# Kernel optimization log

Measured on AMD Instinct MI355X. Metric: run time of the kernel, lower is better.

## Reference

```python
import jax, jax.numpy as jnp
import numpy as np

N = 50000
E = 800000
IN_C = 128
HID = 16
HEADS = 8
OUT_C = 64
NEG_SLOPE = 0.2


def setup_inputs() -> dict:
    key = jax.random.key(0)
    ks = jax.random.split(key, 12)
    x = jax.random.normal(ks[0], (N, IN_C), dtype=jnp.float32)
    edge_index = jax.random.randint(ks[1], (2, E), 0, N, dtype=jnp.int32)
    s = 0.1
    W1 = jax.random.normal(ks[2], (IN_C, HEADS * HID), dtype=jnp.float32) * s
    a1_src = jax.random.normal(ks[3], (HEADS, HID), dtype=jnp.float32) * s
    a1_dst = jax.random.normal(ks[4], (HEADS, HID), dtype=jnp.float32) * s
    b1 = jnp.zeros((HEADS * HID,), dtype=jnp.float32)
    W2 = jax.random.normal(ks[5], (HEADS * HID, OUT_C), dtype=jnp.float32) * s
    a2_src = jax.random.normal(ks[6], (1, OUT_C), dtype=jnp.float32) * s
    a2_dst = jax.random.normal(ks[7], (1, OUT_C), dtype=jnp.float32) * s
    b2 = jnp.zeros((OUT_C,), dtype=jnp.float32)
    return {"x": x, "edge_index": edge_index, "W1": W1, "a1_src": a1_src,
            "a1_dst": a1_dst, "b1": b1, "W2": W2, "a2_src": a2_src,
            "a2_dst": a2_dst, "b2": b2}


def gat_conv(x, src, dst, W, a_src, a_dst, b, heads, ch):
    # linear projection -> [N, H, C]
    h = (x @ W).reshape(N, heads, ch)
    # per-node attention logits [N, H]
    al_s = jnp.einsum('nhc,hc->nh', h, a_src)
    al_d = jnp.einsum('nhc,hc->nh', h, a_dst)
    # per-edge logits [E, H]
    e = jax.nn.leaky_relu(al_s[src] + al_d[dst], NEG_SLOPE)
    # segment softmax over incoming edges of each dst node
    emax = jax.ops.segment_max(e, dst, num_segments=N)
    ee = jnp.exp(e - emax[dst])
    denom = jax.ops.segment_sum(ee, dst, num_segments=N)
    alpha = ee / (denom[dst] + 1e-16)
    # weighted scatter-aggregate of source messages
    msg = h[src] * alpha[:, :, None]  # [E, H, C]
    out = jax.ops.segment_sum(msg, dst, num_segments=N)
    return out.reshape(N, heads * ch) + b


def reference(x, edge_index, W1, a1_src, a1_dst, b1, W2, a2_src, a2_dst, b2):
    # add self loops (PyG GATConv default add_self_loops=True)
    loops = jnp.arange(N, dtype=edge_index.dtype)
    src = jnp.concatenate([edge_index[0], loops])
    dst = jnp.concatenate([edge_index[1], loops])
    h = gat_conv(x, src, dst, W1, a1_src, a1_dst, b1, HEADS, HID)
    h = jax.nn.relu(h)
    # dropout p=0.6 is identity in eval mode
    out = gat_conv(h, src, dst, W2, a2_src, a2_dst, b2, 1, OUT_C)
    return out
```

## Files before the change

### kernel.cpp

```cpp
#include <hip/hip_runtime.h>
#include <hip/hip_fp16.h>
#include <math.h>

#define N_NODES 50000
#define E_EDGES 800000
#define IN_C    128
#define HID     16
#define HEADS   8
#define OUT_C   64
#define NEG_SLOPE 0.2f
#define CELLW   64

typedef _Float16 half8 __attribute__((ext_vector_type(8)));
typedef _Float16 half4 __attribute__((ext_vector_type(4)));
typedef float floatx4 __attribute__((ext_vector_type(4)));

__device__ __forceinline__ float lrelu_exp(float v) {
    v = v > 0.f ? v : NEG_SLOPE * v;
    return __expf(v);
}

__global__ __launch_bounds__(256) void fused_gemm_fill(
    const float* __restrict__ X, const float* __restrict__ W, __half* __restrict__ H,
    const float* __restrict__ a_src, const float* __restrict__ a_dst,
    float* __restrict__ als, float* __restrict__ ald,
    const int* __restrict__ src, const int* __restrict__ dst,
    int* __restrict__ cursor, int* __restrict__ ell) {
    __shared__ _Float16 wT[IN_C * 136];
    const int bid = blockIdx.x;
    const int t = threadIdx.x;

    if (bid & 1) {
        const int tid = (bid >> 1) * 256 + t;
        if (tid < E_EDGES / 4) {
            const int4 s4 = ((const int4*)src)[tid];
            const int4 d4 = ((const int4*)dst)[tid];
            const int p0 = atomicAdd(&cursor[d4.x], 1);
            const int p1 = atomicAdd(&cursor[d4.y], 1);
            const int p2 = atomicAdd(&cursor[d4.z], 1);
            const int p3 = atomicAdd(&cursor[d4.w], 1);
            if (p0 < CELLW) __builtin_nontemporal_store(s4.x, &ell[(size_t)d4.x * CELLW + p0]);
            if (p1 < CELLW) __builtin_nontemporal_store(s4.y, &ell[(size_t)d4.y * CELLW + p1]);
            if (p2 < CELLW) __builtin_nontemporal_store(s4.z, &ell[(size_t)d4.z * CELLW + p2]);
            if (p3 < CELLW) __builtin_nontemporal_store(s4.w, &ell[(size_t)d4.w * CELLW + p3]);
        }
        return;
    }

    {
        const int col = t & 127;
        const int kq = (t >> 7) * 4;
        for (int it = 0; it < 16; ++it) {
            const int k0 = it * 8 + kq;
            half4 hv;
            hv[0] = (_Float16)W[(size_t)(k0 + 0) * IN_C + col];
            hv[1] = (_Float16)W[(size_t)(k0 + 1) * IN_C + col];
            hv[2] = (_Float16)W[(size_t)(k0 + 2) * IN_C + col];
            hv[3] = (_Float16)W[(size_t)(k0 + 3) * IN_C + col];
            *(half4*)&wT[col * 136 + k0] = hv;
        }
    }
    __syncthreads();

    const int wave = t >> 6, lane = t & 63;
    const int m = lane & 15, quad = lane >> 4;
    const int r0w = (bid >> 1) * 64 + wave * 16;
    int rl = r0w + m;
    if (rl >= N_NODES) rl = N_NODES - 1;
    const float* Xr = X + (size_t)rl * IN_C;

    floatx4 acc[8];
#pragma unroll
    for (int i = 0; i < 8; ++i) acc[i] = (floatx4){0.f, 0.f, 0.f, 0.f};

#pragma unroll
    for (int kc = 0; kc < 4; ++kc) {
        const int k8 = kc * 32 + quad * 8;
        const float4 xa = *(const float4*)(Xr + k8);
        const float4 xb = *(const float4*)(Xr + k8 + 4);
        half8 a;
        a[0] = (_Float16)xa.x; a[1] = (_Float16)xa.y;
        a[2] = (_Float16)xa.z; a[3] = (_Float16)xa.w;
        a[4] = (_Float16)xb.x; a[5] = (_Float16)xb.y;
        a[6] = (_Float16)xb.z; a[7] = (_Float16)xb.w;
#pragma unroll
        for (int ct = 0; ct < 8; ++ct) {
            const half8 b = *(const half8*)&wT[(ct * 16 + m) * 136 + k8];
            acc[ct] = __builtin_amdgcn_mfma_f32_16x16x32_f16(a, b, acc[ct], 0, 0, 0);
        }
    }

    _Float16* Hh = (_Float16*)H;
#pragma unroll
    for (int ct = 0; ct < 8; ++ct) {
        const float asv = a_src[ct * 16 + m];
        const float adv = a_dst[ct * 16 + m];
#pragma unroll
        for (int r = 0; r < 4; ++r) {
            const int row = r0w + quad * 4 + r;
            const float c = acc[ct][r];
            float ps = c * asv, pd = c * adv;
            ps += __shfl_xor(ps, 1); pd += __shfl_xor(pd, 1);
            ps += __shfl_xor(ps, 2); pd += __shfl_xor(pd, 2);
            ps += __shfl_xor(ps, 4); pd += __shfl_xor(pd, 4);
            ps += __shfl_xor(ps, 8); pd += __shfl_xor(pd, 8);
            if (row < N_NODES) {
                Hh[(size_t)row * IN_C + ct * 16 + m] = (_Float16)c;
                if (m == 0) {
                    als[(size_t)row * HEADS + ct] = ps;
                    ald[(size_t)row * HEADS + ct] = pd;
                }
            }
        }
    }
}

__global__ __launch_bounds__(256) void agg1_gemm2(
    const int* __restrict__ cnt, const int* __restrict__ ell,
    const float* __restrict__ als, const float* __restrict__ ald,
    const __half* __restrict__ H, const float* __restrict__ b,
    const float* __restrict__ W2, const float* __restrict__ a2_src,
    const float* __restrict__ a2_dst, __half* __restrict__ H2,
    float* __restrict__ als2, float* __restrict__ ald2) {
    __shared__ _Float16 wsh[IN_C * OUT_C];
    __shared__ _Float16 xrowh[32 * 136];
    const int t = threadIdx.x;
    for (int f = t * 4; f < IN_C * OUT_C; f += 1024) {
        const float4 w4 = *(const float4*)&W2[f];
        wsh[f + 0] = (_Float16)w4.x;
        wsh[f + 1] = (_Float16)w4.y;
        wsh[f + 2] = (_Float16)w4.z;
        wsh[f + 3] = (_Float16)w4.w;
    }

    const int nl = t >> 3, h = t & 7;
    int nc = blockIdx.x * 32 + nl;
    if (nc >= N_NODES) nc = N_NODES - 1;
    int deg = cnt[nc];
    deg = deg < CELLW ? deg : CELLW;
    const int* ep = ell + (size_t)nc * CELLW;
    const float ad = ald[nc * HEADS + h];
    float accv[16];
    float ssum;
    {
        const float w = lrelu_exp(als[nc * HEADS + h] + ad);
        const half8* q = (const half8*)(H + ((size_t)nc * HEADS + h) * HID);
        const half8 u0 = q[0], u1 = q[1];
        ssum = w;
#pragma unroll
        for (int j = 0; j < 8; ++j) {
            accv[j] = w * (float)u0[j];
            accv[j + 8] = w * (float)u1[j];
        }
    }
    for (int p = 0; p < deg; p += 4) {
        const int4 s4 = *(const int4*)(ep + p);
        const int s0 = s4.x;
        const int i1 = (p + 1 < deg) ? s4.y : nc;
        const int i2 = (p + 2 < deg) ? s4.z : nc;
        const int i3 = (p + 3 < deg) ? s4.w : nc;
        const float f1 = (p + 1 < deg) ? 1.f : 0.f;
        const float f2 = (p + 2 < deg) ? 1.f : 0.f;
        const float f3 = (p + 3 < deg) ? 1.f : 0.f;
        const float v0 = als[s0 * HEADS + h];
        const float v1 = als[i1 * HEADS + h];
        const float v2 = als[i2 * HEADS + h];
        const float v3 = als[i3 * HEADS + h];
        const half8* q0 = (const half8*)(H + ((size_t)s0 * HEADS + h) * HID);
        const half8* q1 = (const half8*)(H + ((size_t)i1 * HEADS + h) * HID);
        const half8* q2 = (const half8*)(H + ((size_t)i2 * HEADS + h) * HID);
        const half8* q3 = (const half8*)(H + ((size_t)i3 * HEADS + h) * HID);
        const half8 a0 = q0[0], b0 = q0[1];
        const half8 a1 = q1[0], b1 = q1[1];
        const half8 a2 = q2[0], b2 = q2[1];
        const half8 a3 = q3[0], b3 = q3[1];
        const float w0 = lrelu_exp(v0 + ad);
        const float w1 = lrelu_exp(v1 + ad) * f1;
        const float w2 = lrelu_exp(v2 + ad) * f2;
        const float w3 = lrelu_exp(v3 + ad) * f3;
        ssum += (w0 + w1) + (w2 + w3);
#pragma unroll
        for (int j = 0; j < 8; ++j) {
            accv[j]     += w0 * (float)a0[j] + w1 * (float)a1[j] +
                           w2 * (float)a2[j] + w3 * (float)a3[j];
            accv[j + 8] += w0 * (float)b0[j] + w1 * (float)b1[j] +
                           w2 * (float)b2[j] + w3 * (float)b3[j];
        }
    }
    {
        const float inv = 1.f / (ssum + 1e-16f);
        half8 r0, r1;
#pragma unroll
        for (int j = 0; j < 8; ++j) {
            float ra = accv[j] * inv + b[h * 16 + j];
            float rb = accv[j + 8] * inv + b[h * 16 + 8 + j];
            r0[j] = (_Float16)(ra > 0.f ? ra : 0.f);
            r1[j] = (_Float16)(rb > 0.f ? rb : 0.f);
        }
        _Float16* xr = &xrowh[nl * 136 + h * 16];
        *(half8*)(xr) = r0;
        *(half8*)(xr + 8) = r1;
    }

    __syncthreads();

    const int ng = t >> 3, jc = t & 7, j0 = jc * 8;
    const int n2 = blockIdx.x * 32 + ng;
    float o[8] = {};
    const _Float16* xb = &xrowh[ng * 136];
    for (int c8 = 0; c8 < IN_C; c8 += 8) {
        const half8 xv8 = *(const half8*)&xb[c8];
#pragma unroll
        for (int j = 0; j < 8; ++j) {
            const float xv = (float)xv8[j];
            const half8 wv = *(const half8*)&wsh[(c8 + j) * OUT_C + j0];
#pragma unroll
            for (int k = 0; k < 8; ++k) o[k] += xv * (float)wv[k];
        }
    }
    float ps = 0.f, pd = 0.f;
#pragma unroll
    for (int k = 0; k < 8; ++k) {
        ps += o[k] * a2_src[j0 + k];
        pd += o[k] * a2_dst[j0 + k];
    }
    ps += __shfl_xor(ps, 1); pd += __shfl_xor(pd, 1);
    ps += __shfl_xor(ps, 2); pd += __shfl_xor(pd, 2);
    ps += __shfl_xor(ps, 4); pd += __shfl_xor(pd, 4);
    if (n2 < N_NODES) {
        half8 hv;
#pragma unroll
        for (int k = 0; k < 8; ++k) hv[k] = (_Float16)o[k];
        *(half8*)((_Float16*)H2 + (size_t)n2 * OUT_C + j0) = hv;
        if (jc == 0) {
            als2[n2] = ps;
            ald2[n2] = pd;
        }
    }
}

__global__ __launch_bounds__(256) void agg2(
    const int* __restrict__ cnt, const int* __restrict__ ell,
    const float* __restrict__ als, const float* __restrict__ ald,
    const __half* __restrict__ H, const float* __restrict__ b,
    float* __restrict__ out) {
    const int t = threadIdx.x;
    int n = blockIdx.x * 32 + (t >> 3);
    const int j0 = (t & 7) * 8;
    const bool valid = n < N_NODES;
    if (!valid) n = N_NODES - 1;
    int deg = cnt[n];
    deg = deg < CELLW ? deg : CELLW;
    const int* ep = ell + (size_t)n * CELLW;
    const float ad = ald[n];
    float accv[8];
    float ssum;
    {
        const float w = lrelu_exp(als[n] + ad);
        const half8 u = *(const half8*)(H + (size_t)n * OUT_C + j0);
        ssum = w;
#pragma unroll
        for (int k = 0; k < 8; ++k) accv[k] = w * (float)u[k];
    }
    for (int p = 0; p < deg; p += 4) {
        const int4 s4 = *(const int4*)(ep + p);
        const int s0 = s4.x;
        const int i1 = (p + 1 < deg) ? s4.y : n;
        const int i2 = (p + 2 < deg) ? s4.z : n;
        const int i3 = (p + 3 < deg) ? s4.w : n;
        const float f1 = (p + 1 < deg) ? 1.f : 0.f;
        const float f2 = (p + 2 < deg) ? 1.f : 0.f;
        const float f3 = (p + 3 < deg) ? 1.f : 0.f;
        const float v0 = als[s0];
        const float v1 = als[i1];
        const float v2 = als[i2];
        const float v3 = als[i3];
        const half8 u0 = *(const half8*)(H + (size_t)s0 * OUT_C + j0);
        const half8 u1 = *(const half8*)(H + (size_t)i1 * OUT_C + j0);
        const half8 u2 = *(const half8*)(H + (size_t)i2 * OUT_C + j0);
        const half8 u3 = *(const half8*)(H + (size_t)i3 * OUT_C + j0);
        const float w0 = lrelu_exp(v0 + ad);
        const float w1 = lrelu_exp(v1 + ad) * f1;
        const float w2 = lrelu_exp(v2 + ad) * f2;
        const float w3 = lrelu_exp(v3 + ad) * f3;
        ssum += (w0 + w1) + (w2 + w3);
#pragma unroll
        for (int k = 0; k < 8; ++k)
            accv[k] += w0 * (float)u0[k] + w1 * (float)u1[k] +
                       w2 * (float)u2[k] + w3 * (float)u3[k];
    }
    if (valid) {
        const float inv = 1.f / (ssum + 1e-16f);
        floatx4 r0, r1;
        r0[0] = accv[0] * inv + b[j0 + 0]; r0[1] = accv[1] * inv + b[j0 + 1];
        r0[2] = accv[2] * inv + b[j0 + 2]; r0[3] = accv[3] * inv + b[j0 + 3];
        r1[0] = accv[4] * inv + b[j0 + 4]; r1[1] = accv[5] * inv + b[j0 + 5];
        r1[2] = accv[6] * inv + b[j0 + 6]; r1[3] = accv[7] * inv + b[j0 + 7];
        float* op = out + (size_t)n * OUT_C + j0;
        __builtin_nontemporal_store(r0, (floatx4*)op);
        __builtin_nontemporal_store(r1, (floatx4*)(op + 4));
    }
}

extern "C" void kernel_launch(void* const* d_in, const int* in_sizes, int n_in,
                              void* d_out, int out_size, void* d_ws, size_t ws_size,
                              hipStream_t stream) {
    const float* x      = (const float*)d_in[0];
    const int*   ei     = (const int*)d_in[1];
    const float* W1     = (const float*)d_in[2];
    const float* a1_src = (const float*)d_in[3];
    const float* a1_dst = (const float*)d_in[4];
    const float* b1     = (const float*)d_in[5];
    const float* W2     = (const float*)d_in[6];
    const float* a2_src = (const float*)d_in[7];
    const float* a2_dst = (const float*)d_in[8];
    const float* b2     = (const float*)d_in[9];
    const int* src = ei;
    const int* dst = ei + E_EDGES;
    float* outp = (float*)d_out;

    char* wsb = (char*)d_ws;
    __half* h1   = (__half*)wsb;
    __half* h2   = h1 + (size_t)N_NODES * IN_C;
    float*  als1 = (float*)(h2 + (size_t)N_NODES * OUT_C);
    float*  ald1 = als1 + N_NODES * HEADS;
    float*  als2 = ald1 + N_NODES * HEADS;
    float*  ald2 = als2 + N_NODES;
    int*    cursor = (int*)(ald2 + N_NODES);
    int*    ell    = cursor + N_NODES;

    hipMemsetAsync(cursor, 0, N_NODES * sizeof(int), stream);

    {
        const int gemm_blocks = (N_NODES + 63) / 64;
        fused_gemm_fill<<<gemm_blocks * 2, 256, 0, stream>>>(
            x, W1, h1, a1_src, a1_dst, als1, ald1, src, dst, cursor, ell);
    }

    agg1_gemm2<<<(N_NODES + 31) / 32, 256, 0, stream>>>(
        cursor, ell, als1, ald1, h1, b1, W2, a2_src, a2_dst, h2, als2, ald2);

    agg2<<<(N_NODES + 31) / 32, 256, 0, stream>>>(
        cursor, ell, als2, ald2, h2, b2, outp);
}
```

Baseline: 205.3 us.

## Use MFMA f16 instructions for layer-2 projection in agg1_gemm2

Replaces the scalar FMA loop that computes the second-layer projection H2 = relu(h1) @ W2 with MFMA 16x16x32 f16 matrix instructions. W2 is stored transposed in shared memory with padded rows so each lane can load contiguous K slices. The attention logits are reduced with wave shuffles and a small shared buffer, then combined across the two column groups after an extra barrier. This lowers the ALU work of the fused GEMM, at the cost of strided global loads when building the transposed W2 and narrower scattered H2 stores.

```diff
diff --git a/kernel.cpp b/kernel.cpp
--- a/kernel.cpp
+++ b/kernel.cpp
@@ -122,15 +122,22 @@
     const float* __restrict__ W2, const float* __restrict__ a2_src,
     const float* __restrict__ a2_dst, __half* __restrict__ H2,
     float* __restrict__ als2, float* __restrict__ ald2) {
-    __shared__ _Float16 wsh[IN_C * OUT_C];
+    __shared__ _Float16 w2T[OUT_C * 136];
     __shared__ _Float16 xrowh[32 * 136];
+    __shared__ float l2buf[2][32][2];
     const int t = threadIdx.x;
-    for (int f = t * 4; f < IN_C * OUT_C; f += 1024) {
-        const float4 w4 = *(const float4*)&W2[f];
-        wsh[f + 0] = (_Float16)w4.x;
-        wsh[f + 1] = (_Float16)w4.y;
-        wsh[f + 2] = (_Float16)w4.z;
-        wsh[f + 3] = (_Float16)w4.w;
+
+    {
+        const int col = t & 63;
+        const int kg = t >> 6;
+        for (int k0 = kg * 32; k0 < kg * 32 + 32; k0 += 4) {
+            half4 hv;
+            hv[0] = (_Float16)W2[(size_t)(k0 + 0) * OUT_C + col];
+            hv[1] = (_Float16)W2[(size_t)(k0 + 1) * OUT_C + col];
+            hv[2] = (_Float16)W2[(size_t)(k0 + 2) * OUT_C + col];
+            hv[3] = (_Float16)W2[(size_t)(k0 + 3) * OUT_C + col];
+            *(half4*)&w2T[col * 136 + k0] = hv;
+        }
     }
 
     const int nl = t >> 3, h = t & 7;
@@ -204,37 +211,59 @@
 
     __syncthreads();
 
-    const int ng = t >> 3, jc = t & 7, j0 = jc * 8;
-    const int n2 = blockIdx.x * 32 + ng;
-    float o[8] = {};
-    const _Float16* xb = &xrowh[ng * 136];
-    for (int c8 = 0; c8 < IN_C; c8 += 8) {
-        const half8 xv8 = *(const half8*)&xb[c8];
-#pragma unroll
-        for (int j = 0; j < 8; ++j) {
-            const float xv = (float)xv8[j];
-            const half8 wv = *(const half8*)&wsh[(c8 + j) * OUT_C + j0];
-#pragma unroll
-            for (int k = 0; k < 8; ++k) o[k] += xv * (float)wv[k];
-        }
-    }
-    float ps = 0.f, pd = 0.f;
-#pragma unroll
-    for (int k = 0; k < 8; ++k) {
-        ps += o[k] * a2_src[j0 + k];
-        pd += o[k] * a2_dst[j0 + k];
-    }
-    ps += __shfl_xor(ps, 1); pd += __shfl_xor(pd, 1);
-    ps += __shfl_xor(ps, 2); pd += __shfl_xor(pd, 2);
-    ps += __shfl_xor(ps, 4); pd += __shfl_xor(pd, 4);
-    if (n2 < N_NODES) {
-        half8 hv;
-#pragma unroll
-        for (int k = 0; k < 8; ++k) hv[k] = (_Float16)o[k];
-        *(half8*)((_Float16*)H2 + (size_t)n2 * OUT_C + j0) = hv;
-        if (jc == 0) {
-            als2[n2] = ps;
-            ald2[n2] = pd;
+    {
+        const int wv = t >> 6, ln = t & 63;
+        const int bm = ln & 15, quad = ln >> 4;
+        const int mt = wv >> 1;
+        const int ntg = wv & 1;
+        floatx4 acc0 = (floatx4){0.f, 0.f, 0.f, 0.f};
+        floatx4 acc1 = (floatx4){0.f, 0.f, 0.f, 0.f};
+        const _Float16* arow  = &xrowh[(mt * 16 + bm) * 136];
+        const _Float16* brow0 = &w2T[(ntg * 32 + bm) * 136];
+        const _Float16* brow1 = &w2T[(ntg * 32 + 16 + bm) * 136];
+#pragma unroll
+        for (int kc = 0; kc < 4; ++kc) {
+            const int k8 = kc * 32 + quad * 8;
+            const half8 a   = *(const half8*)(arow + k8);
+            const half8 b0v = *(const half8*)(brow0 + k8);
+            const half8 b1v = *(const half8*)(brow1 + k8);
+            acc0 = __builtin_amdgcn_mfma_f32_16x16x32_f16(a, b0v, acc0, 0, 0, 0);
+            acc1 = __builtin_amdgcn_mfma_f32_16x16x32_f16(a, b1v, acc1, 0, 0, 0);
+        }
+        const float a2s0 = a2_src[ntg * 32 + bm],      a2d0 = a2_dst[ntg * 32 + bm];
+        const float a2s1 = a2_src[ntg * 32 + 16 + bm], a2d1 = a2_dst[ntg * 32 + 16 + bm];
+        _Float16* H2h = (_Float16*)H2;
+        float psr[4], pdr[4];
+#pragma unroll
+        for (int r = 0; r < 4; ++r) {
+            const float c0 = acc0[r], c1 = acc1[r];
+            float ps = c0 * a2s0 + c1 * a2s1;
+            float pd = c0 * a2d0 + c1 * a2d1;
+            ps += __shfl_xor(ps, 1); pd += __shfl_xor(pd, 1);
+            ps += __shfl_xor(ps, 2); pd += __shfl_xor(pd, 2);
+            ps += __shfl_xor(ps, 4); pd += __shfl_xor(pd, 4);
+            ps += __shfl_xor(ps, 8); pd += __shfl_xor(pd, 8);
+            psr[r] = ps; pdr[r] = pd;
+            const int row = blockIdx.x * 32 + mt * 16 + quad * 4 + r;
+            if (row < N_NODES) {
+                H2h[(size_t)row * OUT_C + ntg * 32 + bm] = (_Float16)c0;
+                H2h[(size_t)row * OUT_C + ntg * 32 + 16 + bm] = (_Float16)c1;
+            }
+        }
+        if (bm == 0) {
+#pragma unroll
+            for (int r = 0; r < 4; ++r) {
+                l2buf[ntg][mt * 16 + quad * 4 + r][0] = psr[r];
+                l2buf[ntg][mt * 16 + quad * 4 + r][1] = pdr[r];
+            }
+        }
+    }
+    __syncthreads();
+    if (t < 32) {
+        const int n2 = blockIdx.x * 32 + t;
+        if (n2 < N_NODES) {
+            als2[n2] = l2buf[0][t][0] + l2buf[1][t][0];
+            ald2[n2] = l2buf[0][t][1] + l2buf[1][t][1];
         }
     }
 }
```

New measurement: 189.2 us. 1.09x faster.
